# Kernel optimization log

Measured on AMD Instinct MI355X. Metric: run time of the kernel, lower is better.

The kernel has to match this reference:

```python
import jax, jax.numpy as jnp
import numpy as np

D_MODEL, D_STATE, EXPAND = 1024, 32, 2
D_INNER = D_MODEL * EXPAND
B, L = 2, 2048


def setup_inputs() -> dict:
    key = jax.random.key(0)
    ks = jax.random.split(key, 10)
    s = 0.02
    return {
        "x": jax.random.normal(ks[0], (B, L, D_MODEL), dtype=jnp.float32),
        "W_in": jax.random.normal(ks[1], (D_INNER * 2, D_MODEL), dtype=jnp.float32) * s,
        "conv_w": jax.random.normal(ks[2], (D_INNER, 1, 3), dtype=jnp.float32) * 0.3,
        "conv_b": jax.random.normal(ks[3], (D_INNER,), dtype=jnp.float32) * 0.01,
        "A_log": jax.random.normal(ks[4], (D_INNER, D_STATE), dtype=jnp.float32),
        "D_skip": jnp.ones((D_INNER,), dtype=jnp.float32),
        "W_xproj": jax.random.normal(ks[5], (D_STATE * 2 + 1, D_INNER), dtype=jnp.float32) * s,
        "W_dt": jax.random.normal(ks[6], (D_INNER, 1), dtype=jnp.float32) * s,
        "b_dt": jax.random.normal(ks[7], (D_INNER,), dtype=jnp.float32) * 0.01,
        "alpha": jnp.asarray(0.5, dtype=jnp.float32),
        "W_out": jax.random.normal(ks[8], (D_MODEL, D_INNER), dtype=jnp.float32) * s,
    }


def _silu(v):
    return v * jax.nn.sigmoid(v)


def _forward(x, W_in, conv_w, conv_b, A_log, D_skip, W_xproj, W_dt, b_dt, alpha, W_out):
    # in_proj: (B, L, 2*d_inner) -> split into x_in, z
    xz = x @ W_in.T
    x_in, z = jnp.split(xz, 2, axis=-1)

    # depthwise conv1d, kernel 3, padding 1 (same-length, non-causal, as in source)
    xc = jax.lax.conv_general_dilated(
        x_in.transpose(0, 2, 1), conv_w, window_strides=(1,), padding=[(1, 1)],
        dimension_numbers=("NCH", "OIH", "NCH"), feature_group_count=D_INNER,
    ) + conv_b[None, :, None]
    x_conv = _silu(xc.transpose(0, 2, 1))  # (B, L, d_inner)

    # x_proj -> dt_raw (1), B_ssm (N), C_ssm (N)
    proj = x_conv @ W_xproj.T
    dt_raw = proj[..., :1]
    B_ssm = proj[..., 1:1 + D_STATE]
    C_ssm = proj[..., 1 + D_STATE:]
    dt = jax.nn.softplus(dt_raw @ W_dt.T + b_dt)  # (B, L, d_inner)

    A_real = -jnp.exp(A_log)           # (d_inner, d_state)
    a = jax.nn.sigmoid(alpha)

    def step(h, inp):
        dt_t, B_t, C_t, u_t = inp      # (B,d_inner), (B,N), (B,N), (B,d_inner)
        dtA = A_real[None] * dt_t[:, :, None]               # (B, d_inner, N)
        A_d = a * jnp.exp(dtA) + (1.0 - a) / (1.0 - 0.5 * dtA + 1e-6)
        h = A_d * h + (dt_t * u_t)[:, :, None] * B_t[:, None, :]
        y_t = jnp.einsum("bn,bdn->bd", C_t, h) + D_skip * u_t
        return h, y_t

    h0 = jnp.zeros((x.shape[0], D_INNER, D_STATE), dtype=x.dtype)
    xs = (dt.transpose(1, 0, 2), B_ssm.transpose(1, 0, 2),
          C_ssm.transpose(1, 0, 2), x_conv.transpose(1, 0, 2))
    _, ys = jax.lax.scan(step, h0, xs)   # (L, B, d_inner)
    y = ys.transpose(1, 0, 2) * _silu(z)
    return y @ W_out.T


def reference(x, W_in, conv_w, conv_b, A_log, D_skip, W_xproj, W_dt, b_dt, alpha, W_out):
    return _forward(x, W_in, conv_w, conv_b, A_log, D_skip, W_xproj, W_dt, b_dt, alpha, W_out)
```

## Files before the change

### kernel.cpp

```cpp
#include <hip/hip_runtime.h>

#define DM   1024
#define DI   2048
#define DST  32
#define NB   2
#define LSEQ 2048
#define BL   (NB*LSEQ)
#define LC   32
#define NC   64

using bf16   = __bf16;
using bf16x4 = __attribute__((ext_vector_type(4))) __bf16;
using bf16x8 = __attribute__((ext_vector_type(8))) __bf16;
using f32x4  = __attribute__((ext_vector_type(4))) float;
using f16x2  = __attribute__((ext_vector_type(2))) _Float16;

#define AS1(p) ((const __attribute__((address_space(1))) void*)(p))
#define AS3(p) ((__attribute__((address_space(3))) void*)(p))

static __device__ __forceinline__ float sigmoidf_(float x) {
  return 1.f / (1.f + __expf(-x));
}

static __device__ __forceinline__ f16x2 pack_f16x2(float a, float b) {
  return __builtin_bit_cast(f16x2, __builtin_amdgcn_cvt_pkrtz(a, b));
}

static __device__ __forceinline__ float exp2_(float x) {
#if __has_builtin(__builtin_amdgcn_exp2f)
  return __builtin_amdgcn_exp2f(x);
#else
  return exp2f(x);
#endif
}

__global__ __launch_bounds__(256) void cast_bf16_kernel(
    const float* __restrict__ in, bf16* __restrict__ out, int n4) {
  int i = blockIdx.x * 256 + threadIdx.x;
  if (i >= n4) return;
  f32x4 v = ((const f32x4*)in)[i];
  bf16x4 o;
  #pragma unroll
  for (int j = 0; j < 4; ++j) o[j] = (bf16)v[j];
  ((bf16x4*)out)[i] = o;
}

__global__ __launch_bounds__(256) void padcast_wxp_kernel(
    const float* __restrict__ in, bf16* __restrict__ out) {
  int i = blockIdx.x * 256 + threadIdx.x;
  int k4 = i & 511;
  int r  = i >> 9;
  int src = (r < 64) ? (r + 1) : ((r == 127) ? 0 : -1);
  f32x4 v = {0.f, 0.f, 0.f, 0.f};
  if (src >= 0) v = *(const f32x4*)(in + (size_t)src * 2048 + k4 * 4);
  bf16x4 o;
  #pragma unroll
  for (int j = 0; j < 4; ++j) o[j] = (bf16)v[j];
  ((bf16x4*)out)[i] = o;
}

__global__ __launch_bounds__(256) void gemm_lds(
    const bf16* __restrict__ A, const bf16* __restrict__ B,
    float* __restrict__ C, int M, int N, int K, int nz) {
  __shared__ bf16 As2[4][128][8];
  __shared__ bf16 Bs2[4][128][8];

  int tid  = threadIdx.x;
  int bm   = blockIdx.y, bn = blockIdx.x;
  int row0 = bm * 128, col0 = bn * 128;
  int w    = tid >> 6, lane = tid & 63;
  int wr   = w >> 1, wc = w & 1;
  int lr   = lane & 15, lk = lane >> 4;

  int seg = K / nz;
  int kb  = blockIdx.z * seg, ke = kb + seg;
  float* Cz = C + (size_t)blockIdx.z * ((size_t)M * N);

  f32x4 acc[4][4];
  #pragma unroll
  for (int i = 0; i < 4; ++i)
    #pragma unroll
    for (int j = 0; j < 4; ++j) acc[i][j] = f32x4{0.f, 0.f, 0.f, 0.f};

  int j0 = w * 64 + lane, j1 = 256 + w * 64 + lane;
  int ks0 = j0 >> 7, r0s = j0 & 127;
  int ks1 = j1 >> 7, r1s = j1 & 127;
  const bf16* Ag0 = A + (size_t)(row0 + r0s) * K + ks0 * 8;
  const bf16* Ag1 = A + (size_t)(row0 + r1s) * K + ks1 * 8;
  const bf16* Bg0 = B + (size_t)(col0 + r0s) * K + ks0 * 8;
  const bf16* Bg1 = B + (size_t)(col0 + r1s) * K + ks1 * 8;
  bf16* AsL = &As2[0][0][0];
  bf16* BsL = &Bs2[0][0][0];
  int base0 = (w * 64) * 8;
  int base1 = (256 + w * 64) * 8;

  for (int k0 = kb; k0 < ke; k0 += 32) {
    __builtin_amdgcn_global_load_lds(AS1(Ag0 + k0), AS3(AsL + base0), 16, 0, 0);
    __builtin_amdgcn_global_load_lds(AS1(Ag1 + k0), AS3(AsL + base1), 16, 0, 0);
    __builtin_amdgcn_global_load_lds(AS1(Bg0 + k0), AS3(BsL + base0), 16, 0, 0);
    __builtin_amdgcn_global_load_lds(AS1(Bg1 + k0), AS3(BsL + base1), 16, 0, 0);
    __syncthreads();

    bf16x8 af[4], bff[4];
    #pragma unroll
    for (int mi = 0; mi < 4; ++mi)
      af[mi] = *(const bf16x8*)&As2[lk][wr * 64 + mi * 16 + lr][0];
    #pragma unroll
    for (int ni = 0; ni < 4; ++ni)
      bff[ni] = *(const bf16x8*)&Bs2[lk][wc * 64 + ni * 16 + lr][0];

    #pragma unroll
    for (int mi = 0; mi < 4; ++mi)
      #pragma unroll
      for (int ni = 0; ni < 4; ++ni)
        acc[mi][ni] = __builtin_amdgcn_mfma_f32_16x16x32_bf16(
            af[mi], bff[ni], acc[mi][ni], 0, 0, 0);
    __syncthreads();
  }

  #pragma unroll
  for (int mi = 0; mi < 4; ++mi)
    #pragma unroll
    for (int ni = 0; ni < 4; ++ni) {
      int r0 = row0 + wr * 64 + mi * 16 + lk * 4;
      int c  = col0 + wc * 64 + ni * 16 + lr;
      #pragma unroll
      for (int r = 0; r < 4; ++r)
        Cz[(size_t)(r0 + r) * N + c] = acc[mi][ni][r];
    }
}

__global__ __launch_bounds__(256) void reduce_proj_kernel(
    const float* __restrict__ part, float* __restrict__ proj) {
  int i = blockIdx.x * 256 + threadIdx.x;
  f32x4 s = ((const f32x4*)part)[i];
  #pragma unroll
  for (int z = 1; z < 8; ++z) s += ((const f32x4*)part)[(size_t)z * 131072 + i];
  ((f32x4*)proj)[i] = s;
}

__global__ __launch_bounds__(256) void reduce_out_kernel(
    const float* __restrict__ part, float* __restrict__ out) {
  int i = blockIdx.x * 256 + threadIdx.x;
  f32x4 s = ((const f32x4*)part)[i];
  s += ((const f32x4*)part)[(size_t)1048576 + i];
  ((f32x4*)out)[i] = s;
}

__global__ __launch_bounds__(256) void conv_silu_kernel(
    const float* __restrict__ xz, bf16* __restrict__ xconv,
    const float* __restrict__ conv_w, const float* __restrict__ conv_b) {
  int i = blockIdx.x * 256 + threadIdx.x;
  int d4 = i & 511;
  int d  = d4 * 4;
  int bl = i >> 9;
  int l  = bl & (LSEQ - 1);

  const float* base = xz + (size_t)bl * (2 * DI) + d;
  f32x4 zero = {0.f, 0.f, 0.f, 0.f};
  f32x4 xm = (l > 0)        ? *(const f32x4*)(base - 2 * DI) : zero;
  f32x4 xc = *(const f32x4*)(base);
  f32x4 xp = (l < LSEQ - 1) ? *(const f32x4*)(base + 2 * DI) : zero;

  bf16x4 o;
  #pragma unroll
  for (int j = 0; j < 4; ++j) {
    float w0 = conv_w[(d + j) * 3 + 0];
    float w1 = conv_w[(d + j) * 3 + 1];
    float w2 = conv_w[(d + j) * 3 + 2];
    float v = fmaf(w0, xm[j], fmaf(w1, xc[j], fmaf(w2, xp[j], conv_b[d + j])));
    v = v * sigmoidf_(v);
    o[j] = (bf16)v;
  }
  *(bf16x4*)(xconv + (size_t)bl * DI + d) = o;
}


__global__ __launch_bounds__(256, 4) void scan_phase1(
    const float* __restrict__ proj, const bf16* __restrict__ xconv,
    const float* __restrict__ A_log, const float* __restrict__ W_dt,
    const float* __restrict__ b_dt, const float* __restrict__ alpha,
    unsigned int* __restrict__ PH) {
  __shared__ float Bs[LC][32];
  __shared__ bf16  Us[LC][128];
  __shared__ float Ds[LC];
  int tid = threadIdx.x;
  int wid = tid >> 6, lane = tid & 63;
  int dl = lane & 31, nh = lane >> 5;
  int di = wid * 32 + dl;
  int d = blockIdx.x * 128 + di;
  int b = blockIdx.y, c = blockIdx.z;
  int n0 = nh * 16;

  const float* pb = proj + ((size_t)b * LSEQ + c * LC) * 128;
  const bf16*  ub = xconv + ((size_t)b * LSEQ + c * LC) * DI + blockIdx.x * 128;

  {
    const float* g = pb + (size_t)(tid >> 3) * 128 + (tid & 7) * 4;
    __builtin_amdgcn_global_load_lds(AS1(g), AS3((char*)&Bs[0][0] + wid * 1024),
                                     16, 0, 0);
  }
  #pragma unroll
  for (int k = 0; k < 2; ++k) {
    int s = k * 256 + wid * 64 + lane;
    const bf16* g = ub + (size_t)(s >> 4) * DI + (s & 15) * 8;
    __builtin_amdgcn_global_load_lds(AS1(g),
        AS3((char*)&Us[0][0] + (k * 256 + wid * 64) * 16), 16, 0, 0);
  }
  if (tid < LC) Ds[tid] = pb[(size_t)tid * 128 + 127];

  float aG = sigmoidf_(alpha[0]), omA = 1.f - aG;
  float Wd = W_dt[d], bd = b_dt[d];

  float Ar2[16];
  #pragma unroll
  for (int n = 0; n < 16; n += 4) {
    f32x4 al = *(const f32x4*)(A_log + (size_t)d * DST + n0 + n);
    #pragma unroll
    for (int j = 0; j < 4; ++j) Ar2[n + j] = -__expf(al[j]) * 1.44269504f;
  }

  float h[16], P[16];
  #pragma unroll
  for (int n = 0; n < 16; ++n) { h[n] = 0.f; P[n] = 1.f; }

  __syncthreads();

  #pragma unroll 2
  for (int t = 0; t < LC; ++t) {
    float dtraw = Ds[t];
    float u = (float)Us[t][di];
    float s = fmaf(dtraw, Wd, bd);
    float dt = (s > 15.f) ? s : __logf(1.f + __expf(s));
    float dtu = dt * u;
    #pragma unroll
    for (int n4 = 0; n4 < 4; ++n4) {
      f32x4 Bq = *(const f32x4*)&Bs[t][((n0 + n4 * 4) & 31)];
      #pragma unroll
      for (int j = 0; j < 4; ++j) {
        int n = n4 * 4 + j;
        float t1  = dt * Ar2[n];
        float ex  = exp2_(t1);
        float den = fmaf(t1, -0.34657359f, 1.000001f);
        float Ad  = fmaf(aG, ex, omA * __builtin_amdgcn_rcpf(den));
        P[n] *= Ad;
        h[n] = fmaf(Ad, h[n], dtu * Bq[j]);
      }
    }
  }
  size_t ob = (((size_t)c * NB + b) * DI + d) * DST + n0;
  #pragma unroll
  for (int n4 = 0; n4 < 4; ++n4) {
    uint4 o;
    #pragma unroll
    for (int j = 0; j < 4; ++j) {
      int n = n4 * 4 + j;
      ((unsigned int*)&o)[j] =
          __builtin_bit_cast(unsigned int, pack_f16x2(P[n], h[n]));
    }
    *(uint4*)(PH + ob + n4 * 4) = o;
  }
}

__global__ __launch_bounds__(256) void scan_phase2(unsigned int* __restrict__ PH) {
  int i = blockIdx.x * 256 + threadIdx.x;
  float H = 0.f;
  #pragma unroll 4
  for (int c = 0; c < NC; ++c) {
    size_t idx = (size_t)c * (NB * DI * DST) + i;
    f16x2 ph = __builtin_bit_cast(f16x2, PH[idx]);
    ((float*)PH)[idx] = H;
    H = fmaf((float)ph[0], H, (float)ph[1]);
  }
}

__global__ __launch_bounds__(256, 6) void scan_phase3(
    const float* __restrict__ proj, const bf16* __restrict__ xconv,
    const float* __restrict__ xzf,
    const float* __restrict__ A_log, const float* __restrict__ D_skip,
    const float* __restrict__ W_dt, const float* __restrict__ b_dt,
    const float* __restrict__ alpha, const float* __restrict__ PH,
    bf16* __restrict__ yb) {
  __shared__ float    BCs[LC][64];
  __shared__ bf16     Us[LC][128];
  __shared__ _Float16 Gs[LC][128];
  __shared__ float    Ds[LC];
  int tid = threadIdx.x;
  int wid = tid >> 6, lane = tid & 63;
  int dl = lane & 31, nh = lane >> 5;
  int di = wid * 32 + dl;
  int d = blockIdx.x * 128 + di;
  int b = blockIdx.y, c = blockIdx.z;
  int n0 = nh * 16;

  const float* pb = proj + ((size_t)b * LSEQ + c * LC) * 128;
  const bf16*  ub = xconv + ((size_t)b * LSEQ + c * LC) * DI + blockIdx.x * 128;
  const float* zb = xzf + ((size_t)b * LSEQ + c * LC) * 4096 + 2048
                    + blockIdx.x * 128;

  {
    const float* g0 = pb + (size_t)(tid >> 4) * 128 + (tid & 15) * 4;
    int s1 = tid + 256;
    const float* g1 = pb + (size_t)(s1 >> 4) * 128 + (s1 & 15) * 4;
    char* base = (char*)&BCs[0][0];
    __builtin_amdgcn_global_load_lds(AS1(g0), AS3(base + wid * 1024), 16, 0, 0);
    __builtin_amdgcn_global_load_lds(AS1(g1), AS3(base + 4096 + wid * 1024),
                                     16, 0, 0);
  }
  #pragma unroll
  for (int k = 0; k < 2; ++k) {
    int s = k * 256 + wid * 64 + lane;
    const bf16* g = ub + (size_t)(s >> 4) * DI + (s & 15) * 8;
    __builtin_amdgcn_global_load_lds(AS1(g),
        AS3((char*)&Us[0][0] + (k * 256 + wid * 64) * 16), 16, 0, 0);
  }
  #pragma unroll
  for (int k = 0; k < 4; ++k) {
    int s = k * 256 + tid;
    int row = s >> 5, q = s & 31;
    f32x4 z = *(const f32x4*)(zb + (size_t)row * 4096 + q * 4);
    uint2 o;
    o.x = __builtin_bit_cast(unsigned int,
          pack_f16x2(z[0] * sigmoidf_(z[0]), z[1] * sigmoidf_(z[1])));
    o.y = __builtin_bit_cast(unsigned int,
          pack_f16x2(z[2] * sigmoidf_(z[2]), z[3] * sigmoidf_(z[3])));
    *(uint2*)&Gs[row][q * 4] = o;
  }
  if (tid < LC) Ds[tid] = pb[(size_t)tid * 128 + 127];

  float aG = sigmoidf_(alpha[0]), omA = 1.f - aG;
  float Dsk = D_skip[d];
  float Wd = W_dt[d], bd = b_dt[d];

  float Ar2[16];
  #pragma unroll
  for (int n = 0; n < 16; n += 4) {
    f32x4 al = *(const f32x4*)(A_log + (size_t)d * DST + n0 + n);
    #pragma unroll
    for (int j = 0; j < 4; ++j) Ar2[n + j] = -__expf(al[j]) * 1.44269504f;
  }

  float h[16];
  size_t ob = (((size_t)c * NB + b) * DI + d) * DST + n0;
  #pragma unroll
  for (int n = 0; n < 16; n += 4) {
    f32x4 hv = *(const f32x4*)(PH + ob + n);
    #pragma unroll
    for (int j = 0; j < 4; ++j) h[n + j] = hv[j];
  }

  bf16* yc = yb + ((size_t)b * LSEQ + c * LC) * DI + d;

  __syncthreads();

  #pragma unroll 2
  for (int t = 0; t < LC; ++t) {
    float dtraw = Ds[t];
    float u = (float)Us[t][di];
    float s = fmaf(dtraw, Wd, bd);
    float dt = (s > 15.f) ? s : __logf(1.f + __expf(s));
    float dtu = dt * u;
    float p0 = 0.f, p1 = 0.f, p2 = 0.f, p3 = 0.f;
    #pragma unroll
    for (int n4 = 0; n4 < 4; ++n4) {
      f32x4 Bq = *(const f32x4*)&BCs[t][n0 + n4 * 4];
      f32x4 Cq = *(const f32x4*)&BCs[t][32 + n0 + n4 * 4];
      #pragma unroll
      for (int j = 0; j < 4; ++j) {
        int n = n4 * 4 + j;
        float t1  = dt * Ar2[n];
        float ex  = exp2_(t1);
        float den = fmaf(t1, -0.34657359f, 1.000001f);
        float Ad  = fmaf(aG, ex, omA * __builtin_amdgcn_rcpf(den));
        h[n] = fmaf(Ad, h[n], dtu * Bq[j]);
        if (j == 0)      p0 = fmaf(Cq[j], h[n], p0);
        else if (j == 1) p1 = fmaf(Cq[j], h[n], p1);
        else if (j == 2) p2 = fmaf(Cq[j], h[n], p2);
        else             p3 = fmaf(Cq[j], h[n], p3);
      }
    }
    float part = (p0 + p1) + (p2 + p3);
    part += __shfl_xor(part, 32);
    if (nh == 0) {
      float g = (float)Gs[t][di];
      float y = fmaf(Dsk, u, part) * g;
      yc[(size_t)t * DI] = (bf16)y;
    }
  }
}

extern "C" void kernel_launch(void* const* d_in, const int* in_sizes, int n_in,
                              void* d_out, int out_size, void* d_ws, size_t ws_size,
                              hipStream_t stream) {
  const float* x      = (const float*)d_in[0];
  const float* W_in   = (const float*)d_in[1];
  const float* conv_w = (const float*)d_in[2];
  const float* conv_b = (const float*)d_in[3];
  const float* A_log  = (const float*)d_in[4];
  const float* D_skip = (const float*)d_in[5];
  const float* W_xprj = (const float*)d_in[6];
  const float* W_dt   = (const float*)d_in[7];
  const float* b_dt   = (const float*)d_in[8];
  const float* alpha  = (const float*)d_in[9];
  const float* W_out  = (const float*)d_in[10];

  char* ws = (char*)d_ws;
  float* xz    = (float*)(ws + 0);
  bf16*  xconv = (bf16*) (ws + 67108864);
  float* proj  = (float*)(ws + 83886080);
  bf16*  woutb = (bf16*) (ws + 85983232);
  bf16*  wxpb  = (bf16*) (ws + 90177536);
  bf16*  yb    = (bf16*) (ws + 90701824);
  unsigned int* PH = (unsigned int*)(ws + 107479040);
  bf16*  xb    = (bf16*) (ws + 107479040);
  bf16*  winb  = (bf16*) (ws + 115867648);
  float* projp = (float*)(ws + 107479040);
  float* outp  = (float*)(ws + 107479040);

  float* out = (float*)d_out;

  cast_bf16_kernel<<<4096, 256, 0, stream>>>(x, xb, BL * DM / 4);
  cast_bf16_kernel<<<4096, 256, 0, stream>>>(W_in, winb, 2 * DI * DM / 4);
  cast_bf16_kernel<<<2048, 256, 0, stream>>>(W_out, woutb, DM * DI / 4);
  padcast_wxp_kernel<<<256, 256, 0, stream>>>(W_xprj, wxpb);

  gemm_lds<<<dim3(32, 32, 1), 256, 0, stream>>>(xb, winb, xz, BL, 2 * DI, DM, 1);

  conv_silu_kernel<<<8192, 256, 0, stream>>>(xz, xconv, conv_w, conv_b);

  gemm_lds<<<dim3(1, 32, 8), 256, 0, stream>>>(xconv, wxpb, projp, BL, 128, DI, 8);
  reduce_proj_kernel<<<512, 256, 0, stream>>>(projp, proj);

  scan_phase1<<<dim3(DI / 128, NB, NC - 1), 256, 0, stream>>>(proj, xconv,
                                                              A_log, W_dt,
                                                              b_dt, alpha, PH);
  scan_phase2<<<512, 256, 0, stream>>>(PH);
  scan_phase3<<<dim3(DI / 128, NB, NC), 256, 0, stream>>>(proj, xconv, xz,
                                                          A_log, D_skip, W_dt,
                                                          b_dt, alpha,
                                                          (const float*)PH, yb);

  gemm_lds<<<dim3(8, 32, 2), 256, 0, stream>>>(yb, woutb, outp, BL, DM, DI, 2);
  reduce_out_kernel<<<4096, 256, 0, stream>>>(outp, out);
}
```

Baseline: 363.1 us.

## Store in_proj output as bf16 and merge weight cast kernels

The in_proj GEMM now writes its xz output in bf16 instead of fp32, and both the conv kernel and the z-gate load in scan_phase3 read bf16. This halves the traffic for the large intermediate written once and read twice. The four separate cast kernels are also merged into one prep launch to cut launch overhead. In exchange, x_in and z are rounded to bf16 before the conv and the gating, which adds some precision loss.

```diff
diff --git a/kernel.cpp b/kernel.cpp
--- a/kernel.cpp
+++ b/kernel.cpp
@@ -34,34 +34,46 @@
 #endif
 }
 
-__global__ __launch_bounds__(256) void cast_bf16_kernel(
-    const float* __restrict__ in, bf16* __restrict__ out, int n4) {
-  int i = blockIdx.x * 256 + threadIdx.x;
-  if (i >= n4) return;
-  f32x4 v = ((const f32x4*)in)[i];
-  bf16x4 o;
-  #pragma unroll
-  for (int j = 0; j < 4; ++j) o[j] = (bf16)v[j];
-  ((bf16x4*)out)[i] = o;
-}
-
-__global__ __launch_bounds__(256) void padcast_wxp_kernel(
-    const float* __restrict__ in, bf16* __restrict__ out) {
-  int i = blockIdx.x * 256 + threadIdx.x;
-  int k4 = i & 511;
-  int r  = i >> 9;
-  int src = (r < 64) ? (r + 1) : ((r == 127) ? 0 : -1);
-  f32x4 v = {0.f, 0.f, 0.f, 0.f};
-  if (src >= 0) v = *(const f32x4*)(in + (size_t)src * 2048 + k4 * 4);
-  bf16x4 o;
-  #pragma unroll
-  for (int j = 0; j < 4; ++j) o[j] = (bf16)v[j];
-  ((bf16x4*)out)[i] = o;
-}
-
+__global__ __launch_bounds__(256) void prep_kernel(
+    const float* __restrict__ x, const float* __restrict__ W_in,
+    const float* __restrict__ W_out, const float* __restrict__ W_xprj,
+    bf16* __restrict__ xb, bf16* __restrict__ winb,
+    bf16* __restrict__ woutb, bf16* __restrict__ wxpb) {
+  int blk = blockIdx.x;
+  if (blk < 8192) {
+    const float* in; bf16* out; int i;
+    if (blk < 4096) { in = x; out = xb; i = blk * 256 + threadIdx.x; }
+    else { in = W_in; out = winb; i = (blk - 4096) * 256 + threadIdx.x; }
+    f32x4 v = ((const f32x4*)in)[i];
+    bf16x4 o;
+    #pragma unroll
+    for (int j = 0; j < 4; ++j) o[j] = (bf16)v[j];
+    ((bf16x4*)out)[i] = o;
+  } else if (blk < 10240) {
+    int i = (blk - 8192) * 256 + threadIdx.x;
+    f32x4 v = ((const f32x4*)W_out)[i];
+    bf16x4 o;
+    #pragma unroll
+    for (int j = 0; j < 4; ++j) o[j] = (bf16)v[j];
+    ((bf16x4*)woutb)[i] = o;
+  } else {
+    int i = (blk - 10240) * 256 + threadIdx.x;
+    int k4 = i & 511;
+    int r  = i >> 9;
+    int src = (r < 64) ? (r + 1) : ((r == 127) ? 0 : -1);
+    f32x4 v = {0.f, 0.f, 0.f, 0.f};
+    if (src >= 0) v = *(const f32x4*)(W_xprj + (size_t)src * 2048 + k4 * 4);
+    bf16x4 o;
+    #pragma unroll
+    for (int j = 0; j < 4; ++j) o[j] = (bf16)v[j];
+    ((bf16x4*)wxpb)[i] = o;
+  }
+}
+
+template <typename CT>
 __global__ __launch_bounds__(256) void gemm_lds(
     const bf16* __restrict__ A, const bf16* __restrict__ B,
-    float* __restrict__ C, int M, int N, int K, int nz) {
+    CT* __restrict__ C, int M, int N, int K, int nz) {
   __shared__ bf16 As2[4][128][8];
   __shared__ bf16 Bs2[4][128][8];
 
@@ -74,7 +86,7 @@
 
   int seg = K / nz;
   int kb  = blockIdx.z * seg, ke = kb + seg;
-  float* Cz = C + (size_t)blockIdx.z * ((size_t)M * N);
+  CT* Cz = C + (size_t)blockIdx.z * ((size_t)M * N);
 
   f32x4 acc[4][4];
   #pragma unroll
@@ -126,7 +138,7 @@
       int c  = col0 + wc * 64 + ni * 16 + lr;
       #pragma unroll
       for (int r = 0; r < 4; ++r)
-        Cz[(size_t)(r0 + r) * N + c] = acc[mi][ni][r];
+        Cz[(size_t)(r0 + r) * N + c] = (CT)acc[mi][ni][r];
     }
 }
 
@@ -148,7 +160,7 @@
 }
 
 __global__ __launch_bounds__(256) void conv_silu_kernel(
-    const float* __restrict__ xz, bf16* __restrict__ xconv,
+    const bf16* __restrict__ xzb, bf16* __restrict__ xconv,
     const float* __restrict__ conv_w, const float* __restrict__ conv_b) {
   int i = blockIdx.x * 256 + threadIdx.x;
   int d4 = i & 511;
@@ -156,11 +168,11 @@
   int bl = i >> 9;
   int l  = bl & (LSEQ - 1);
 
-  const float* base = xz + (size_t)bl * (2 * DI) + d;
-  f32x4 zero = {0.f, 0.f, 0.f, 0.f};
-  f32x4 xm = (l > 0)        ? *(const f32x4*)(base - 2 * DI) : zero;
-  f32x4 xc = *(const f32x4*)(base);
-  f32x4 xp = (l < LSEQ - 1) ? *(const f32x4*)(base + 2 * DI) : zero;
+  const bf16* base = xzb + (size_t)bl * (2 * DI) + d;
+  bf16x4 zero4 = {(bf16)0.f, (bf16)0.f, (bf16)0.f, (bf16)0.f};
+  bf16x4 xm = (l > 0)        ? *(const bf16x4*)(base - 2 * DI) : zero4;
+  bf16x4 xc = *(const bf16x4*)(base);
+  bf16x4 xp = (l < LSEQ - 1) ? *(const bf16x4*)(base + 2 * DI) : zero4;
 
   bf16x4 o;
   #pragma unroll
@@ -168,7 +180,9 @@
     float w0 = conv_w[(d + j) * 3 + 0];
     float w1 = conv_w[(d + j) * 3 + 1];
     float w2 = conv_w[(d + j) * 3 + 2];
-    float v = fmaf(w0, xm[j], fmaf(w1, xc[j], fmaf(w2, xp[j], conv_b[d + j])));
+    float v = fmaf(w0, (float)xm[j],
+              fmaf(w1, (float)xc[j],
+              fmaf(w2, (float)xp[j], conv_b[d + j])));
     v = v * sigmoidf_(v);
     o[j] = (bf16)v;
   }
@@ -276,7 +290,7 @@
 
 __global__ __launch_bounds__(256, 6) void scan_phase3(
     const float* __restrict__ proj, const bf16* __restrict__ xconv,
-    const float* __restrict__ xzf,
+    const bf16* __restrict__ xzb,
     const float* __restrict__ A_log, const float* __restrict__ D_skip,
     const float* __restrict__ W_dt, const float* __restrict__ b_dt,
     const float* __restrict__ alpha, const float* __restrict__ PH,
@@ -295,7 +309,7 @@
 
   const float* pb = proj + ((size_t)b * LSEQ + c * LC) * 128;
   const bf16*  ub = xconv + ((size_t)b * LSEQ + c * LC) * DI + blockIdx.x * 128;
-  const float* zb = xzf + ((size_t)b * LSEQ + c * LC) * 4096 + 2048
+  const bf16*  zb = xzb + ((size_t)b * LSEQ + c * LC) * (2 * DI) + 2048
                     + blockIdx.x * 128;
 
   {
@@ -315,16 +329,18 @@
         AS3((char*)&Us[0][0] + (k * 256 + wid * 64) * 16), 16, 0, 0);
   }
   #pragma unroll
-  for (int k = 0; k < 4; ++k) {
+  for (int k = 0; k < 2; ++k) {
     int s = k * 256 + tid;
-    int row = s >> 5, q = s & 31;
-    f32x4 z = *(const f32x4*)(zb + (size_t)row * 4096 + q * 4);
-    uint2 o;
-    o.x = __builtin_bit_cast(unsigned int,
-          pack_f16x2(z[0] * sigmoidf_(z[0]), z[1] * sigmoidf_(z[1])));
-    o.y = __builtin_bit_cast(unsigned int,
-          pack_f16x2(z[2] * sigmoidf_(z[2]), z[3] * sigmoidf_(z[3])));
-    *(uint2*)&Gs[row][q * 4] = o;
+    int row = s >> 4, oct = s & 15;
+    bf16x8 zv = *(const bf16x8*)(zb + (size_t)row * (2 * DI) + oct * 8);
+    uint4 o;
+    #pragma unroll
+    for (int q = 0; q < 4; ++q) {
+      float z0 = (float)zv[2 * q], z1 = (float)zv[2 * q + 1];
+      ((unsigned int*)&o)[q] = __builtin_bit_cast(unsigned int,
+          pack_f16x2(z0 * sigmoidf_(z0), z1 * sigmoidf_(z1)));
+    }
+    *(uint4*)&Gs[row][oct * 8] = o;
   }
   if (tid < LC) Ds[tid] = pb[(size_t)tid * 128 + 127];
 
@@ -405,7 +421,7 @@
   const float* W_out  = (const float*)d_in[10];
 
   char* ws = (char*)d_ws;
-  float* xz    = (float*)(ws + 0);
+  bf16*  xzb   = (bf16*) (ws + 0);
   bf16*  xconv = (bf16*) (ws + 67108864);
   float* proj  = (float*)(ws + 83886080);
   bf16*  woutb = (bf16*) (ws + 85983232);
@@ -419,27 +435,28 @@
 
   float* out = (float*)d_out;
 
-  cast_bf16_kernel<<<4096, 256, 0, stream>>>(x, xb, BL * DM / 4);
-  cast_bf16_kernel<<<4096, 256, 0, stream>>>(W_in, winb, 2 * DI * DM / 4);
-  cast_bf16_kernel<<<2048, 256, 0, stream>>>(W_out, woutb, DM * DI / 4);
-  padcast_wxp_kernel<<<256, 256, 0, stream>>>(W_xprj, wxpb);
-
-  gemm_lds<<<dim3(32, 32, 1), 256, 0, stream>>>(xb, winb, xz, BL, 2 * DI, DM, 1);
-
-  conv_silu_kernel<<<8192, 256, 0, stream>>>(xz, xconv, conv_w, conv_b);
-
-  gemm_lds<<<dim3(1, 32, 8), 256, 0, stream>>>(xconv, wxpb, projp, BL, 128, DI, 8);
+  prep_kernel<<<10496, 256, 0, stream>>>(x, W_in, W_out, W_xprj,
+                                         xb, winb, woutb, wxpb);
+
+  gemm_lds<bf16><<<dim3(32, 32, 1), 256, 0, stream>>>(xb, winb, xzb,
+                                                      BL, 2 * DI, DM, 1);
+
+  conv_silu_kernel<<<8192, 256, 0, stream>>>(xzb, xconv, conv_w, conv_b);
+
+  gemm_lds<float><<<dim3(1, 32, 8), 256, 0, stream>>>(xconv, wxpb, projp,
+                                                      BL, 128, DI, 8);
   reduce_proj_kernel<<<512, 256, 0, stream>>>(projp, proj);
 
   scan_phase1<<<dim3(DI / 128, NB, NC - 1), 256, 0, stream>>>(proj, xconv,
                                                               A_log, W_dt,
                                                               b_dt, alpha, PH);
   scan_phase2<<<512, 256, 0, stream>>>(PH);
-  scan_phase3<<<dim3(DI / 128, NB, NC), 256, 0, stream>>>(proj, xconv, xz,
+  scan_phase3<<<dim3(DI / 128, NB, NC), 256, 0, stream>>>(proj, xconv, xzb,
                                                           A_log, D_skip, W_dt,
                                                           b_dt, alpha,
                                                           (const float*)PH, yb);
 
-  gemm_lds<<<dim3(8, 32, 2), 256, 0, stream>>>(yb, woutb, outp, BL, DM, DI, 2);
+  gemm_lds<float><<<dim3(8, 32, 2), 256, 0, stream>>>(yb, woutb, outp,
+                                                      BL, DM, DI, 2);
   reduce_out_kernel<<<4096, 256, 0, stream>>>(outp, out);
 }
```

Result: faster. 350.2 us (-3.6%).
